# Kernel optimization log

Measured on AMD Instinct MI355X. Metric: run time of the kernel, lower is better.

## Reference

```python
import jax, jax.numpy as jnp
import numpy as np

N_NODES = 50000
N_EDGES = 1600000
IN_FEAT = 48
OUT_FEAT = 48
NUM_RELS = 8


def setup_inputs() -> dict:
    key = jax.random.key(0)
    ks = jax.random.split(key, 9)
    # xavier-ish scale for relu gain
    s1 = float(np.sqrt(2.0) * np.sqrt(6.0 / (IN_FEAT + IN_FEAT)))
    s2 = float(np.sqrt(2.0) * np.sqrt(6.0 / (IN_FEAT + OUT_FEAT)))
    return {
        "inputs": jax.random.normal(ks[0], (N_NODES, IN_FEAT), dtype=jnp.float32),
        "norm": jax.random.uniform(ks[1], (N_EDGES, 1), dtype=jnp.float32),
        "weight1": jax.random.uniform(ks[2], (NUM_RELS, IN_FEAT, IN_FEAT), jnp.float32, -s1, s1),
        "weight2": jax.random.uniform(ks[3], (NUM_RELS, IN_FEAT, OUT_FEAT), jnp.float32, -s2, s2),
        "bias1": jax.random.normal(ks[4], (IN_FEAT,), dtype=jnp.float32) * 0.1,
        "bias2": jax.random.normal(ks[5], (OUT_FEAT,), dtype=jnp.float32) * 0.1,
        "src": jax.random.randint(ks[6], (N_EDGES,), 0, N_NODES, dtype=jnp.int64) if jax.config.jax_enable_x64 else jax.random.randint(ks[6], (N_EDGES,), 0, N_NODES).astype(jnp.int32),
        "dst": jax.random.randint(ks[7], (N_EDGES,), 0, N_NODES).astype(jnp.int32),
        "rel_type": jax.random.randint(ks[8], (N_EDGES,), 0, NUM_RELS).astype(jnp.int32),
    }


def reference(inputs, norm, weight1, weight2, bias1, bias2, src, dst, rel_type):
    # Message depends only on (src node, relation): precompute per (node, rel).
    # Stage 1: h1[n,r,:] = relu(h[n] @ W1[r] + b1)   -> [N, R, in]
    h1 = jax.nn.relu(jnp.einsum('ni,rij->nrj', inputs, weight1) + bias1)
    # Stage 2: h2[n,r,:] = h1[n,r] @ W2[r]           -> [N, R, out]
    h2 = jnp.einsum('nrj,rjo->nro', h1, weight2)
    # Per-edge gather + norm scaling                 -> [E, out]
    msg = h2[src, rel_type] * norm
    # Scatter-sum aggregation to destination nodes   -> [N, out]
    agg = jax.ops.segment_sum(msg, dst, num_segments=inputs.shape[0])
    # apply_func: bias2 + activation
    return jax.nn.relu(agg + bias2)
```

## Files before the change

### kernel.cpp

```cpp
#include <hip/hip_runtime.h>

#define NN 50000
#define EE 1600000
#define FF 48
#define RR 8
#define H2_ROW 64
#define LSTR 72
#define CAP 96

#define WB 8

#define H2TILES 391
#define H2BLKS (H2TILES * RR)
#define K2GRID (H2BLKS * 3)

typedef __attribute__((ext_vector_type(8))) short frag8;
typedef __attribute__((ext_vector_type(4))) float frag4f;

__device__ inline unsigned short bf16r(float f) {
    unsigned u = __float_as_uint(f);
    return (unsigned short)((u + 0x7FFFu + ((u >> 16) & 1u)) >> 16);
}
__device__ inline unsigned bf16pack2(float a, float b) {
    return (unsigned)bf16r(a) | ((unsigned)bf16r(b) << 16);
}
__device__ inline frag8 pack8(float4 a, float4 b) {
    union { frag8 f; unsigned u[4]; } r;
    r.u[0] = bf16pack2(a.x, a.y); r.u[1] = bf16pack2(a.z, a.w);
    r.u[2] = bf16pack2(b.x, b.y); r.u[3] = bf16pack2(b.z, b.w);
    return r.f;
}

__global__ __launch_bounds__(256) void pre_kernel(
    const float* __restrict__ W1, const float* __restrict__ W2,
    unsigned short* __restrict__ W1t, unsigned short* __restrict__ W2t)
{
    int r = blockIdx.x;
    const float* w1 = W1 + (size_t)r * FF * FF;
    const float* w2 = W2 + (size_t)r * FF * FF;
    for (int idx = threadIdx.x; idx < 48 * 64; idx += 256) {
        int j = idx >> 6, k = idx & 63;
        W1t[(size_t)r * 48 * 64 + idx] = (k < FF) ? bf16r(w1[k * FF + j]) : (unsigned short)0;
        W2t[(size_t)r * 48 * 64 + idx] = (k < FF) ? bf16r(w2[k * FF + j]) : (unsigned short)0;
    }
}

__global__ __launch_bounds__(256) void h2_place_kernel(
    const float* __restrict__ X, const unsigned short* __restrict__ W1t,
    const unsigned short* __restrict__ W2t, const float* __restrict__ B1,
    const int* __restrict__ srcv, const int* __restrict__ dstv,
    const int* __restrict__ relv, const float* __restrict__ norm,
    int* __restrict__ count, unsigned* __restrict__ payload,
    unsigned short* __restrict__ H2)
{
    __shared__ unsigned short h1s[128 * LSTR];
    int b = blockIdx.x;
    int bmod = b - (b / 3) * 3;
    if (bmod != 0) {
        int p = (b / 3) * 2 + bmod - 1;
        int e = p * 256 + threadIdx.x;
        if (e < EE) {
            int d = dstv[e];
            int pos = atomicAdd(&count[d], 1);
            unsigned qn = (unsigned)(norm[e] * 8192.0f + 0.5f);
            if (qn > 8191u) qn = 8191u;
            unsigned rec = ((unsigned)(srcv[e] * 8 + relv[e]) << 13) | qn;
            if ((unsigned)pos < (unsigned)CAP)
                __builtin_nontemporal_store(rec, &payload[(size_t)d * CAP + pos]);
        }
        return;
    }
    int h    = b / 3;
    int r    = h & 7;
    int tile = h >> 3;
    int tid  = threadIdx.x;
    int w    = tid >> 6, ln = tid & 63, q = ln >> 4, lq = ln & 15;
    int nb   = tile * 128 + w * 32;

    unsigned short* myh1 = &h1s[(w * 32) * LSTR];
    for (int i = ln; i < 32 * 12; i += 64) {
        int rr = i / 12, cs = i - rr * 12;
        *(unsigned*)&myh1[rr * LSTR + 48 + cs * 2] = 0;
    }

    int row0 = nb + lq;      if (row0 >= NN) row0 = NN - 1;
    int row1 = nb + 16 + lq; if (row1 >= NN) row1 = NN - 1;
    const float* x0 = X + (size_t)row0 * FF;
    const float* x1 = X + (size_t)row1 * FF;

    frag8 a00 = pack8(*(const float4*)(x0 + q * 8), *(const float4*)(x0 + q * 8 + 4));
    frag8 a10 = pack8(*(const float4*)(x1 + q * 8), *(const float4*)(x1 + q * 8 + 4));
    frag8 a01 = {0, 0, 0, 0, 0, 0, 0, 0};
    frag8 a11 = {0, 0, 0, 0, 0, 0, 0, 0};
    if (q < 2) {
        a01 = pack8(*(const float4*)(x0 + 32 + q * 8), *(const float4*)(x0 + 36 + q * 8));
        a11 = pack8(*(const float4*)(x1 + 32 + q * 8), *(const float4*)(x1 + 36 + q * 8));
    }

    const unsigned short* w1r = W1t + (size_t)r * 48 * 64;
    const unsigned short* w2r = W2t + (size_t)r * 48 * 64;

    #pragma unroll
    for (int t = 0; t < 3; ++t) {
        int col = t * 16 + lq;
        frag8 b0 = *(const frag8*)&w1r[(col << 6) + q * 8];
        frag8 b1 = *(const frag8*)&w1r[(col << 6) + 32 + q * 8];
        float bc = B1[col];
        frag4f acc0 = {bc, bc, bc, bc};
        frag4f acc1 = {bc, bc, bc, bc};
        acc0 = __builtin_amdgcn_mfma_f32_16x16x32_bf16(a00, b0, acc0, 0, 0, 0);
        acc0 = __builtin_amdgcn_mfma_f32_16x16x32_bf16(a01, b1, acc0, 0, 0, 0);
        acc1 = __builtin_amdgcn_mfma_f32_16x16x32_bf16(a10, b0, acc1, 0, 0, 0);
        acc1 = __builtin_amdgcn_mfma_f32_16x16x32_bf16(a11, b1, acc1, 0, 0, 0);
        #pragma unroll
        for (int g = 0; g < 4; ++g) {
            myh1[(q * 4 + g) * LSTR + col]      = bf16r(fmaxf(acc0[g], 0.0f));
            myh1[(16 + q * 4 + g) * LSTR + col] = bf16r(fmaxf(acc1[g], 0.0f));
        }
    }

    const frag8 c00 = *(const frag8*)&myh1[lq * LSTR + q * 8];
    const frag8 c01 = *(const frag8*)&myh1[lq * LSTR + 32 + q * 8];
    const frag8 c10 = *(const frag8*)&myh1[(16 + lq) * LSTR + q * 8];
    const frag8 c11 = *(const frag8*)&myh1[(16 + lq) * LSTR + 32 + q * 8];

    #pragma unroll
    for (int t = 0; t < 3; ++t) {
        int col = t * 16 + lq;
        frag8 b0 = *(const frag8*)&w2r[(col << 6) + q * 8];
        frag8 b1 = *(const frag8*)&w2r[(col << 6) + 32 + q * 8];
        frag4f acc0 = {0.f, 0.f, 0.f, 0.f};
        frag4f acc1 = {0.f, 0.f, 0.f, 0.f};
        acc0 = __builtin_amdgcn_mfma_f32_16x16x32_bf16(c00, b0, acc0, 0, 0, 0);
        acc0 = __builtin_amdgcn_mfma_f32_16x16x32_bf16(c01, b1, acc0, 0, 0, 0);
        acc1 = __builtin_amdgcn_mfma_f32_16x16x32_bf16(c10, b0, acc1, 0, 0, 0);
        acc1 = __builtin_amdgcn_mfma_f32_16x16x32_bf16(c11, b1, acc1, 0, 0, 0);
        #pragma unroll
        for (int g = 0; g < 4; ++g) {
            int n0 = nb + q * 4 + g;
            int n1 = nb + 16 + q * 4 + g;
            if (n0 < NN) H2[((size_t)n0 * RR + r) * H2_ROW + col] = bf16r(acc0[g]);
            if (n1 < NN) H2[((size_t)n1 * RR + r) * H2_ROW + col] = bf16r(acc1[g]);
        }
    }
}

__global__ __launch_bounds__(256) void gather_kernel(
    const unsigned short* __restrict__ H2, const unsigned* __restrict__ payload,
    const int* __restrict__ count, const float* __restrict__ B2,
    float* __restrict__ out)
{
    unsigned tid = blockIdx.x * 256u + threadIdx.x;
    unsigned n = tid / 12u;
    unsigned c = tid - n * 12u;
    if (n >= NN) return;

    int cnt = count[n];
    if (cnt > CAP) cnt = CAP;
    if (cnt < 0) cnt = 0;
    const unsigned* pl = payload + (size_t)n * CAP;
    float a0 = 0.f, a1 = 0.f, a2 = 0.f, a3 = 0.f;

    int e = 0;
    for (; e + 16 <= cnt; e += 16) {
        unsigned p[16];
        #pragma unroll
        for (int k = 0; k < 16; ++k) p[k] = pl[e + k];
        uint2 v[16];
        #pragma unroll
        for (int k = 0; k < 16; ++k)
            v[k] = ((const uint2*)(H2 + (size_t)(p[k] >> 13) * H2_ROW))[c];
        #pragma unroll
        for (int k = 0; k < 16; ++k) {
            float nm = (float)(p[k] & 8191u) * (1.0f / 8192.0f);
            a0 = fmaf(__uint_as_float(v[k].x << 16),         nm, a0);
            a1 = fmaf(__uint_as_float(v[k].x & 0xFFFF0000u), nm, a1);
            a2 = fmaf(__uint_as_float(v[k].y << 16),         nm, a2);
            a3 = fmaf(__uint_as_float(v[k].y & 0xFFFF0000u), nm, a3);
        }
    }
    for (; e + 8 <= cnt; e += 8) {
        unsigned p[8];
        #pragma unroll
        for (int k = 0; k < 8; ++k) p[k] = pl[e + k];
        uint2 v[8];
        #pragma unroll
        for (int k = 0; k < 8; ++k)
            v[k] = ((const uint2*)(H2 + (size_t)(p[k] >> 13) * H2_ROW))[c];
        #pragma unroll
        for (int k = 0; k < 8; ++k) {
            float nm = (float)(p[k] & 8191u) * (1.0f / 8192.0f);
            a0 = fmaf(__uint_as_float(v[k].x << 16),         nm, a0);
            a1 = fmaf(__uint_as_float(v[k].x & 0xFFFF0000u), nm, a1);
            a2 = fmaf(__uint_as_float(v[k].y << 16),         nm, a2);
            a3 = fmaf(__uint_as_float(v[k].y & 0xFFFF0000u), nm, a3);
        }
    }
    for (; e < cnt; ++e) {
        unsigned p = pl[e];
        float nm = (float)(p & 8191u) * (1.0f / 8192.0f);
        uint2 v = ((const uint2*)(H2 + (size_t)(p >> 13) * H2_ROW))[c];
        a0 = fmaf(__uint_as_float(v.x << 16),         nm, a0);
        a1 = fmaf(__uint_as_float(v.x & 0xFFFF0000u), nm, a1);
        a2 = fmaf(__uint_as_float(v.y << 16),         nm, a2);
        a3 = fmaf(__uint_as_float(v.y & 0xFFFF0000u), nm, a3);
    }
    float4 b = ((const float4*)B2)[c];
    ((float4*)out)[(size_t)n * 12u + c] = make_float4(
        fmaxf(a0 + b.x, 0.f), fmaxf(a1 + b.y, 0.f),
        fmaxf(a2 + b.z, 0.f), fmaxf(a3 + b.w, 0.f));
}

extern "C" void kernel_launch(void* const* d_in, const int* in_sizes, int n_in,
                              void* d_out, int out_size, void* d_ws, size_t ws_size,
                              hipStream_t stream) {
    const float* X   = (const float*)d_in[0];
    const float* nrm = (const float*)d_in[1];
    const float* W1  = (const float*)d_in[2];
    const float* W2  = (const float*)d_in[3];
    const float* B1  = (const float*)d_in[4];
    const float* B2  = (const float*)d_in[5];
    const int*   src = (const int*)d_in[6];
    const int*   dst = (const int*)d_in[7];
    const int*   rel = (const int*)d_in[8];
    float* out = (float*)d_out;

    unsigned short* H2      = (unsigned short*)d_ws;
    unsigned*       payload = (unsigned*)(H2 + (size_t)NN * RR * H2_ROW);
    unsigned short* W1t     = (unsigned short*)(payload + (size_t)NN * CAP);
    unsigned short* W2t     = W1t + RR * 48 * 64;
    int*            count   = (int*)(W2t + RR * 48 * 64);

    hipMemsetAsync(count, 0, (size_t)NN * sizeof(int), stream);

    pre_kernel<<<WB, 256, 0, stream>>>(W1, W2, W1t, W2t);

    h2_place_kernel<<<K2GRID, 256, 0, stream>>>(
        X, W1t, W2t, B1, src, dst, rel, nrm, count, payload, H2);

    unsigned total = (unsigned)NN * 12u;
    gather_kernel<<<(total + 255) / 256, 256, 0, stream>>>(
        H2, payload, count, B2, out);
}
```

Before: 228.3 us.

## Split per-node edge buckets into per-XCD segments to localize atomics

Replaces the single per-destination counter and 96-slot payload bucket with 8 sub-buckets of 16 slots, one per XCD (picked by reading the XCC_ID hardware register), with linear probing into other segments on overflow. The intent is to keep atomic counter updates local to each XCD's L2 instead of contending across dies. The gather kernel now loads 8 counts, computes prefix offsets, and maps each edge index to a segment slot through a branchy lookup; the 16-wide unrolled loop is removed. The count array grows eightfold, and the per-edge address computation and the extra probing atomics add cost.

```diff
diff --git a/kernel.cpp b/kernel.cpp
--- a/kernel.cpp
+++ b/kernel.cpp
@@ -6,7 +6,8 @@
 #define RR 8
 #define H2_ROW 64
 #define LSTR 72
-#define CAP 96
+#define NSEG 8
+#define SCAP 16
 
 #define WB 8
 
@@ -60,13 +61,24 @@
         int p = (b / 3) * 2 + bmod - 1;
         int e = p * 256 + threadIdx.x;
         if (e < EE) {
+            int xcd;
+            asm volatile("s_getreg_b32 %0, hwreg(HW_REG_XCC_ID)" : "=s"(xcd));
+            xcd &= (NSEG - 1);
             int d = dstv[e];
-            int pos = atomicAdd(&count[d], 1);
             unsigned qn = (unsigned)(norm[e] * 8192.0f + 0.5f);
             if (qn > 8191u) qn = 8191u;
             unsigned rec = ((unsigned)(srcv[e] * 8 + relv[e]) << 13) | qn;
-            if ((unsigned)pos < (unsigned)CAP)
-                __builtin_nontemporal_store(rec, &payload[(size_t)d * CAP + pos]);
+            int x = xcd;
+            #pragma unroll 1
+            for (int attempt = 0; attempt < NSEG; ++attempt) {
+                int pos = atomicAdd(&count[d * NSEG + x], 1);
+                if (pos < SCAP) {
+                    __builtin_nontemporal_store(
+                        rec, &payload[((size_t)d * NSEG + x) * SCAP + pos]);
+                    break;
+                }
+                x = (x + 1) & (NSEG - 1);
+            }
         }
         return;
     }
@@ -155,34 +167,35 @@
     unsigned c = tid - n * 12u;
     if (n >= NN) return;
 
-    int cnt = count[n];
-    if (cnt > CAP) cnt = CAP;
-    if (cnt < 0) cnt = 0;
-    const unsigned* pl = payload + (size_t)n * CAP;
+    int4 ca = ((const int4*)(count + (size_t)n * NSEG))[0];
+    int4 cb = ((const int4*)(count + (size_t)n * NSEG))[1];
+    int c0 = min(ca.x, SCAP), c1 = min(ca.y, SCAP);
+    int c2 = min(ca.z, SCAP), c3 = min(ca.w, SCAP);
+    int c4 = min(cb.x, SCAP), c5 = min(cb.y, SCAP);
+    int c6 = min(cb.z, SCAP), c7 = min(cb.w, SCAP);
+    int p1 = c0, p2 = p1 + c1, p3 = p2 + c2, p4 = p3 + c3;
+    int p5 = p4 + c4, p6 = p5 + c5, p7 = p6 + c6;
+    int total = p7 + c7;
+    const unsigned* pl = payload + (size_t)n * (NSEG * SCAP);
+
+    auto slot = [&](int idx) -> unsigned {
+        int x, base;
+        if (idx < p4) {
+            if (idx < p2) { x = (idx < p1) ? 0 : 1; base = (idx < p1) ? 0 : p1; }
+            else          { x = (idx < p3) ? 2 : 3; base = (idx < p3) ? p2 : p3; }
+        } else {
+            if (idx < p6) { x = (idx < p5) ? 4 : 5; base = (idx < p5) ? p4 : p5; }
+            else          { x = (idx < p7) ? 6 : 7; base = (idx < p7) ? p6 : p7; }
+        }
+        return pl[x * SCAP + (idx - base)];
+    };
+
     float a0 = 0.f, a1 = 0.f, a2 = 0.f, a3 = 0.f;
-
     int e = 0;
-    for (; e + 16 <= cnt; e += 16) {
-        unsigned p[16];
-        #pragma unroll
-        for (int k = 0; k < 16; ++k) p[k] = pl[e + k];
-        uint2 v[16];
-        #pragma unroll
-        for (int k = 0; k < 16; ++k)
-            v[k] = ((const uint2*)(H2 + (size_t)(p[k] >> 13) * H2_ROW))[c];
-        #pragma unroll
-        for (int k = 0; k < 16; ++k) {
-            float nm = (float)(p[k] & 8191u) * (1.0f / 8192.0f);
-            a0 = fmaf(__uint_as_float(v[k].x << 16),         nm, a0);
-            a1 = fmaf(__uint_as_float(v[k].x & 0xFFFF0000u), nm, a1);
-            a2 = fmaf(__uint_as_float(v[k].y << 16),         nm, a2);
-            a3 = fmaf(__uint_as_float(v[k].y & 0xFFFF0000u), nm, a3);
-        }
-    }
-    for (; e + 8 <= cnt; e += 8) {
+    for (; e + 8 <= total; e += 8) {
         unsigned p[8];
         #pragma unroll
-        for (int k = 0; k < 8; ++k) p[k] = pl[e + k];
+        for (int k = 0; k < 8; ++k) p[k] = slot(e + k);
         uint2 v[8];
         #pragma unroll
         for (int k = 0; k < 8; ++k)
@@ -196,8 +209,8 @@
             a3 = fmaf(__uint_as_float(v[k].y & 0xFFFF0000u), nm, a3);
         }
     }
-    for (; e < cnt; ++e) {
-        unsigned p = pl[e];
+    for (; e < total; ++e) {
+        unsigned p = slot(e);
         float nm = (float)(p & 8191u) * (1.0f / 8192.0f);
         uint2 v = ((const uint2*)(H2 + (size_t)(p >> 13) * H2_ROW))[c];
         a0 = fmaf(__uint_as_float(v.x << 16),         nm, a0);
@@ -227,11 +240,11 @@
 
     unsigned short* H2      = (unsigned short*)d_ws;
     unsigned*       payload = (unsigned*)(H2 + (size_t)NN * RR * H2_ROW);
-    unsigned short* W1t     = (unsigned short*)(payload + (size_t)NN * CAP);
+    unsigned short* W1t     = (unsigned short*)(payload + (size_t)NN * NSEG * SCAP);
     unsigned short* W2t     = W1t + RR * 48 * 64;
     int*            count   = (int*)(W2t + RR * 48 * 64);
 
-    hipMemsetAsync(count, 0, (size_t)NN * sizeof(int), stream);
+    hipMemsetAsync(count, 0, (size_t)NN * NSEG * sizeof(int), stream);
 
     pre_kernel<<<WB, 256, 0, stream>>>(W1, W2, W1t, W2t);
 
```

New measurement: 218.0 us. 4.5% less time.
